# Kernel optimization log

Hardware: AMD Instinct MI355X
Metric: run time of the kernel (lower is better)

Reference implementation:

```python
import jax, jax.numpy as jnp
import numpy as np

BANDWIDTH = 1.0  # init kwarg: bandwidth; sphere mode -> var_s = gamma = bandwidth
LOG2PI = float(np.log(2.0 * np.pi))


def setup_inputs() -> dict:
    key = jax.random.key(0)
    k1, k2, k3, k4 = jax.random.split(key, 4)
    x = jax.random.normal(k1, (4096, 256), dtype=jnp.float32)
    y = jax.random.normal(k2, (4096, 128), dtype=jnp.float32)
    x_s = jax.random.normal(k3, (8192, 256), dtype=jnp.float32)
    y_s = jax.random.normal(k4, (8192, 128), dtype=jnp.float32)
    return {"x": x, "y": y, "x_s": x_s, "y_s": y_s}


def _sq_dists(a, b):
    # ||a_i - b_j||^2 via GEMM expansion: (batch, num_s)
    a2 = jnp.sum(a * a, axis=-1)[:, None]
    b2 = jnp.sum(b * b, axis=-1)[None, :]
    return a2 + b2 - 2.0 * jnp.einsum("bd,sd->bs", a, b)


def reference(x, y, x_s, y_s):
    x_dim = x.shape[-1]
    y_dim = y.shape[-1]
    var_s = BANDWIDTH
    gamma = BANDWIDTH
    logA_x = x_dim * (LOG2PI + jnp.log(jnp.float32(var_s)))
    logA_y = y_dim * (LOG2PI + jnp.log(jnp.float32(gamma)))

    sdx = _sq_dists(x, x_s) / var_s  # (batch, num_s)
    sdy = _sq_dists(y, y_s) / gamma  # (batch, num_s)

    E_log_pxy = jax.nn.logsumexp(-0.5 * (logA_x + logA_y + sdx + sdy), axis=-1)
    E_log_px = jax.nn.logsumexp(-0.5 * (logA_x + sdx), axis=-1)
    E_log_py = jax.nn.logsumexp(-0.5 * (logA_y + sdy), axis=-1)
    return jnp.mean(E_log_pxy - E_log_px - E_log_py)
```

## Files before the change

kernel.cpp:

```cpp
#include <hip/hip_runtime.h>
#include <hip/hip_bf16.h>
#include <stdint.h>

#define B_N 4096
#define S_N 8192
#define KX  256
#define KY  128
#define BM 128
#define BN 128

typedef __bf16 bf16x8 __attribute__((ext_vector_type(8)));
typedef float  f32x4  __attribute__((ext_vector_type(4)));

#define OFF_XH   ((size_t)0)
#define OFF_YH   ((size_t)2097152)
#define OFF_SXH  ((size_t)3145728)
#define OFF_SYH  ((size_t)7340032)
#define OFF_NX   ((size_t)9437184)
#define OFF_NY   (OFF_NX + 16384)
#define OFF_NSX  (OFF_NY + 16384)
#define OFF_NSY  (OFF_NSX + 32768)
#define OFF_PART (OFF_NSY + 32768)
#define OFF_BSUM (OFF_PART + (size_t)3*64*4096*2*4)

__device__ __forceinline__ void gl2lds16(const void* g, void* l) {
  typedef const __attribute__((address_space(1))) unsigned int* gp_t;
  typedef __attribute__((address_space(3))) unsigned int* lp_t;
  __builtin_amdgcn_global_load_lds((gp_t)g, (lp_t)l, 16, 0, 0);
}

__device__ __forceinline__ unsigned short f2bf(float f) {
  unsigned u = __builtin_bit_cast(unsigned, f);
  return (unsigned short)((u + 0x7fffu + ((u >> 16) & 1u)) >> 16);
}

__global__ __launch_bounds__(256) void conv_all(const float* __restrict__ x,
                                                const float* __restrict__ y,
                                                const float* __restrict__ xs,
                                                const float* __restrict__ ys,
                                                char* __restrict__ ws) {
  int b    = blockIdx.x;
  int wave = threadIdx.x >> 6;
  int lane = threadIdx.x & 63;
  const float* src; unsigned short* hi; float* nrm;
  int K, row;
  if (b < 1024) {
    src = x;  hi = (unsigned short*)(ws + OFF_XH);
    nrm = (float*)(ws + OFF_NX); K = 256; row = b * 4 + wave;
  } else if (b < 2048) {
    src = y;  hi = (unsigned short*)(ws + OFF_YH);
    nrm = (float*)(ws + OFF_NY); K = 128; row = (b - 1024) * 4 + wave;
  } else if (b < 4096) {
    src = xs; hi = (unsigned short*)(ws + OFF_SXH);
    nrm = (float*)(ws + OFF_NSX); K = 256; row = (b - 2048) * 4 + wave;
  } else {
    src = ys; hi = (unsigned short*)(ws + OFF_SYH);
    nrm = (float*)(ws + OFF_NSY); K = 128; row = (b - 4096) * 4 + wave;
  }
  float acc = 0.f;
  if (K == 256) {
    float4 v = ((const float4*)(src + (size_t)row * 256))[lane];
    float vv[4] = {v.x, v.y, v.z, v.w};
    ushort4 h4;
    unsigned short* hp = (unsigned short*)&h4;
    #pragma unroll
    for (int k = 0; k < 4; ++k) {
      hp[k] = f2bf(vv[k]);
      acc = fmaf(vv[k], vv[k], acc);
    }
    ((ushort4*)(hi + (size_t)row * 256))[lane] = h4;
  } else {
    float2 v = ((const float2*)(src + (size_t)row * 128))[lane];
    float vv[2] = {v.x, v.y};
    ushort2 h2;
    unsigned short* hp = (unsigned short*)&h2;
    #pragma unroll
    for (int k = 0; k < 2; ++k) {
      hp[k] = f2bf(vv[k]);
      acc = fmaf(vv[k], vv[k], acc);
    }
    ((ushort2*)(hi + (size_t)row * 128))[lane] = h2;
  }
  #pragma unroll
  for (int o = 32; o > 0; o >>= 1) acc += __shfl_down(acc, o);
  if (lane == 0) nrm[row] = acc;
}

__global__ __launch_bounds__(512, 4) void mie_main(const char* __restrict__ ws,
                                                   float* __restrict__ part) {
  __shared__ __align__(16) char smem[65536];

  const int tid  = threadIdx.x;
  const int lane = tid & 63;
  const int wave = tid >> 6;
  const int c    = lane & 15;
  const int q    = lane >> 4;
  const int wm   = wave >> 1;
  const int wn   = wave & 1;

  const int b     = blockIdx.x;
  const int xcd   = b & 7;
  const int w     = b >> 3;
  const int bm_t  = w & 31;
  const int sn_t  = xcd * 8 + (w >> 5);
  const int bm0   = bm_t * BM;
  const int sn0   = sn_t * BN;

  const char* xh  = ws + OFF_XH;
  const char* yh  = ws + OFF_YH;
  const char* sxh = ws + OFF_SXH;
  const char* syh = ws + OFF_SYH;
  const float* nx  = (const float*)(ws + OFF_NX);
  const float* ny  = (const float*)(ws + OFF_NY);
  const float* nsx = (const float*)(ws + OFF_NSX);
  const float* nsy = (const float*)(ws + OFF_NSY);

  const int r  = tid >> 2;
  const int sg = (tid & 3) ^ ((r >> 1) & 3);
  const char* aXp = xh  + (size_t)(bm0 + r) * 512 + sg * 16;
  const char* aYp = yh  + (size_t)(bm0 + r) * 256 + sg * 16;
  const char* bXp = sxh + (size_t)(sn0 + r) * 512 + sg * 16;
  const char* bYp = syh + (size_t)(sn0 + r) * 256 + sg * 16;
  char* sdst = smem + wave * 1024;

  const int slot  = (q ^ ((c >> 1) & 3)) * 16;
  const int aoff0 = (wm * 32 +  0 + c) * 64 + slot;
  const int aoff1 = (wm * 32 + 16 + c) * 64 + slot;
  const int boff0 = (wn * 64 +  0 + c) * 64 + slot;
  const int boff1 = (wn * 64 + 16 + c) * 64 + slot;
  const int boff2 = (wn * 64 + 32 + c) * 64 + slot;
  const int boff3 = (wn * 64 + 48 + c) * 64 + slot;

  f32x4 accx[2][4], accy[2][4];
  #pragma unroll
  for (int i = 0; i < 2; ++i)
    #pragma unroll
    for (int j = 0; j < 4; ++j) {
      accx[i][j] = (f32x4){0.f,0.f,0.f,0.f};
      accy[i][j] = (f32x4){0.f,0.f,0.f,0.f};
    }

#define STAGE(kc) do {                                                      \
    const char* _sa; const char* _sb;                                       \
    if ((kc) < 8) { _sa = aXp + (kc) * 64;       _sb = bXp + (kc) * 64; }   \
    else          { _sa = aYp + ((kc) - 8) * 64; _sb = bYp + ((kc) - 8) * 64; } \
    char* _d = sdst + ((kc) & 3) * 16384;                                   \
    gl2lds16(_sa, _d);                                                      \
    gl2lds16(_sb, _d + 8192);                                               \
  } while (0)

#define MFMA8(ACC, A0, A1, B0, B1, B2, B3) do {                                   \
    ACC[0][0] = __builtin_amdgcn_mfma_f32_16x16x32_bf16(A0, B0, ACC[0][0], 0,0,0); \
    ACC[0][1] = __builtin_amdgcn_mfma_f32_16x16x32_bf16(A0, B1, ACC[0][1], 0,0,0); \
    ACC[0][2] = __builtin_amdgcn_mfma_f32_16x16x32_bf16(A0, B2, ACC[0][2], 0,0,0); \
    ACC[0][3] = __builtin_amdgcn_mfma_f32_16x16x32_bf16(A0, B3, ACC[0][3], 0,0,0); \
    ACC[1][0] = __builtin_amdgcn_mfma_f32_16x16x32_bf16(A1, B0, ACC[1][0], 0,0,0); \
    ACC[1][1] = __builtin_amdgcn_mfma_f32_16x16x32_bf16(A1, B1, ACC[1][1], 0,0,0); \
    ACC[1][2] = __builtin_amdgcn_mfma_f32_16x16x32_bf16(A1, B2, ACC[1][2], 0,0,0); \
    ACC[1][3] = __builtin_amdgcn_mfma_f32_16x16x32_bf16(A1, B3, ACC[1][3], 0,0,0); \
  } while (0)

#define ITER(kc, vm, ACC) do {                                              \
    asm volatile("s_waitcnt vmcnt(" #vm ")" ::: "memory");                  \
    __builtin_amdgcn_s_barrier();                                           \
    asm volatile("" ::: "memory");                                          \
    const char* _base = smem + ((kc) & 3) * 16384;                          \
    bf16x8 _A0 = *(const bf16x8*)(_base + aoff0);                           \
    bf16x8 _A1 = *(const bf16x8*)(_base + aoff1);                           \
    bf16x8 _B0 = *(const bf16x8*)(_base + 8192 + boff0);                    \
    bf16x8 _B1 = *(const bf16x8*)(_base + 8192 + boff1);                    \
    bf16x8 _B2 = *(const bf16x8*)(_base + 8192 + boff2);                    \
    bf16x8 _B3 = *(const bf16x8*)(_base + 8192 + boff3);                    \
    if ((kc) + 3 < 12) STAGE((kc) + 3);                                     \
    __builtin_amdgcn_s_setprio(1);                                          \
    MFMA8(ACC, _A0, _A1, _B0, _B1, _B2, _B3);                               \
    __builtin_amdgcn_s_setprio(0);                                          \
  } while (0)

  STAGE(0); STAGE(1); STAGE(2);

  ITER(0, 4, accx);  ITER(1, 4, accx);  ITER(2, 4, accx);  ITER(3, 4, accx);
  ITER(4, 4, accx);  ITER(5, 4, accx);  ITER(6, 4, accx);  ITER(7, 4, accx);
  ITER(8, 4, accy);  ITER(9, 4, accy);  ITER(10, 2, accy); ITER(11, 0, accy);

#undef ITER
#undef MFMA8
#undef STAGE

  float hxv[2][4], hyv[2][4];
  #pragma unroll
  for (int i = 0; i < 2; ++i)
    #pragma unroll
    for (int rr4 = 0; rr4 < 4; ++rr4) {
      int rr = bm0 + wm * 32 + i * 16 + q * 4 + rr4;
      hxv[i][rr4] = -0.5f * nx[rr];
      hyv[i][rr4] = -0.5f * ny[rr];
    }
  float hsxv[4], hsyv[4];
  #pragma unroll
  for (int j = 0; j < 4; ++j) {
    int cc = sn0 + wn * 64 + j * 16 + c;
    hsxv[j] = -0.5f * nsx[cc];
    hsyv[j] = -0.5f * nsy[cc];
  }

  float2* xch2 = (float2*)smem;
  #pragma unroll
  for (int i = 0; i < 2; ++i) {
    #pragma unroll
    for (int rr4 = 0; rr4 < 4; ++rr4) {
      float vx[4], vy[4];
      #pragma unroll
      for (int j = 0; j < 4; ++j) {
        vx[j] = accx[i][j][rr4] + hxv[i][rr4] + hsxv[j];
        vy[j] = accy[i][j][rr4] + hyv[i][rr4] + hsyv[j];
      }
      int rl = wm * 32 + i * 16 + q * 4 + rr4;
      #pragma unroll
      for (int st = 0; st < 3; ++st) {
        float v0 = (st == 0) ? vx[0] + vy[0] : (st == 1 ? vx[0] : vy[0]);
        float v1 = (st == 0) ? vx[1] + vy[1] : (st == 1 ? vx[1] : vy[1]);
        float v2 = (st == 0) ? vx[2] + vy[2] : (st == 1 ? vx[2] : vy[2]);
        float v3 = (st == 0) ? vx[3] + vy[3] : (st == 1 ? vx[3] : vy[3]);
        float m = fmaxf(fmaxf(v0, v1), fmaxf(v2, v3));
        float s = __expf(v0 - m) + __expf(v1 - m) + __expf(v2 - m) + __expf(v3 - m);
        float mo = __shfl_xor(m, 8);
        float so = __shfl_xor(s, 8);
        float nm = fmaxf(m, mo);
        float ns = s * __expf(m - nm) + so * __expf(mo - nm);
        if (c < 8) xch2[(st * 128 + rl) * 16 + wn * 8 + c] = (float2){nm, ns};
      }
    }
  }
  __syncthreads();

  if (tid < 384) {
    int st = tid >> 7;
    int rl = tid & 127;
    const float2* row = xch2 + (st * 128 + rl) * 16;
    int p0 = rl & 15;
    float2 a = row[p0];
    float m = a.x, s = a.y;
    #pragma unroll
    for (int p = 1; p < 16; ++p) {
      float2 e = row[(p0 + p) & 15];
      float nm = fmaxf(m, e.x);
      s = s * __expf(m - nm) + e.y * __expf(e.x - nm);
      m = nm;
    }
    size_t idx = ((size_t)st * 64 + sn_t) * B_N + (bm0 + rl);
    ((float2*)part)[idx] = (float2){m, s};
  }
}

__global__ __launch_bounds__(256) void fin1(const float* __restrict__ part,
                                            float* __restrict__ bsum) {
  __shared__ float2 lds[3][4][64];
  int tid  = threadIdx.x;
  int wave = tid >> 6;
  int lane = tid & 63;
  int row  = blockIdx.x * 64 + lane;
  #pragma unroll
  for (int j = 0; j < 3; ++j) {
    float m = -__builtin_inff(), s = 0.f;
    #pragma unroll
    for (int pp = 0; pp < 16; ++pp) {
      int p = wave * 16 + pp;
      float2 a = ((const float2*)part)[((size_t)j * 64 + p) * B_N + row];
      float nm = fmaxf(m, a.x);
      s = s * __expf(m - nm) + a.y * __expf(a.x - nm);
      m = nm;
    }
    lds[j][wave][lane] = (float2){m, s};
  }
  __syncthreads();
  if (wave == 0) {
    float v[3];
    #pragma unroll
    for (int j = 0; j < 3; ++j) {
      float m = -__builtin_inff(), s = 0.f;
      #pragma unroll
      for (int u = 0; u < 4; ++u) {
        float2 a = lds[j][u][lane];
        float nm = fmaxf(m, a.x);
        s = s * __expf(m - nm) + a.y * __expf(a.x - nm);
        m = nm;
      }
      v[j] = m + __logf(s);
    }
    float local = v[0] - v[1] - v[2];
    #pragma unroll
    for (int o = 32; o > 0; o >>= 1) local += __shfl_down(local, o);
    if (lane == 0) bsum[blockIdx.x] = local;
  }
}

__global__ void fin2(const float* __restrict__ bsum, float* __restrict__ out) {
  int t = threadIdx.x;
  float a = bsum[t];
  #pragma unroll
  for (int o = 32; o > 0; o >>= 1) a += __shfl_down(a, o);
  if (t == 0) out[0] = a * (1.0f / (float)B_N);
}

extern "C" void kernel_launch(void* const* d_in, const int* in_sizes, int n_in,
                              void* d_out, int out_size, void* d_ws, size_t ws_size,
                              hipStream_t stream) {
  (void)in_sizes; (void)n_in; (void)out_size; (void)ws_size;
  const float* x  = (const float*)d_in[0];
  const float* y  = (const float*)d_in[1];
  const float* xs = (const float*)d_in[2];
  const float* ys = (const float*)d_in[3];
  char* ws = (char*)d_ws;

  conv_all<<<6144, 256, 0, stream>>>(x, y, xs, ys, ws);
  mie_main<<<2048, 512, 0, stream>>>(ws, (float*)(ws + OFF_PART));
  fin1<<<B_N / 64, 256, 0, stream>>>((const float*)(ws + OFF_PART), (float*)(ws + OFF_BSUM));
  fin2<<<1, 64, 0, stream>>>((const float*)(ws + OFF_BSUM), (float*)d_out);
}
```

Baseline: 130.5 us.

## Load A fragments straight to registers and fuse final reductions via atomic last-block

The A operand is now loaded from global memory directly into registers with one-step lookahead instead of being staged through LDS. This cuts LDS to 48KB and halves the global-to-LDS traffic per stage. The two finishing kernels are replaced by a last-block-done pattern: atomic counters per row panel pick the final block, which merges the partial logsumexp values, and a global counter does the final mean. This removes two kernel launches at the cost of atomics, fences and more per-thread global loads that are not shared across waves.

```diff
diff --git a/kernel.cpp b/kernel.cpp
--- a/kernel.cpp
+++ b/kernel.cpp
@@ -42,6 +42,7 @@
   int b    = blockIdx.x;
   int wave = threadIdx.x >> 6;
   int lane = threadIdx.x & 63;
+  if (b == 0 && threadIdx.x < 34) ((unsigned*)(ws + OFF_BSUM))[threadIdx.x] = 0u;
   const float* src; unsigned short* hi; float* nrm;
   int K, row;
   if (b < 1024) {
@@ -86,9 +87,11 @@
   if (lane == 0) nrm[row] = acc;
 }
 
-__global__ __launch_bounds__(512, 4) void mie_main(const char* __restrict__ ws,
-                                                   float* __restrict__ part) {
-  __shared__ __align__(16) char smem[65536];
+__global__ __launch_bounds__(512, 4) void mie_main(char* __restrict__ ws,
+                                                   float* __restrict__ part,
+                                                   float* __restrict__ out) {
+  __shared__ __align__(16) char smem[49152];
+  __shared__ int lastFlag;
 
   const int tid  = threadIdx.x;
   const int lane = tid & 63;
@@ -114,18 +117,20 @@
   const float* ny  = (const float*)(ws + OFF_NY);
   const float* nsx = (const float*)(ws + OFF_NSX);
   const float* nsy = (const float*)(ws + OFF_NSY);
+  unsigned* cnt_panel = (unsigned*)(ws + OFF_BSUM);
+  unsigned* done      = cnt_panel + 32;
+  float*    fsum      = (float*)(cnt_panel + 33);
 
   const int r  = tid >> 2;
   const int sg = (tid & 3) ^ ((r >> 1) & 3);
-  const char* aXp = xh  + (size_t)(bm0 + r) * 512 + sg * 16;
-  const char* aYp = yh  + (size_t)(bm0 + r) * 256 + sg * 16;
   const char* bXp = sxh + (size_t)(sn0 + r) * 512 + sg * 16;
   const char* bYp = syh + (size_t)(sn0 + r) * 256 + sg * 16;
   char* sdst = smem + wave * 1024;
 
+  const char* aXb = xh + (size_t)(bm0 + wm * 32 + c) * 512 + q * 16;
+  const char* aYb = yh + (size_t)(bm0 + wm * 32 + c) * 256 + q * 16;
+
   const int slot  = (q ^ ((c >> 1) & 3)) * 16;
-  const int aoff0 = (wm * 32 +  0 + c) * 64 + slot;
-  const int aoff1 = (wm * 32 + 16 + c) * 64 + slot;
   const int boff0 = (wn * 64 +  0 + c) * 64 + slot;
   const int boff1 = (wn * 64 + 16 + c) * 64 + slot;
   const int boff2 = (wn * 64 + 32 + c) * 64 + slot;
@@ -140,13 +145,21 @@
       accy[i][j] = (f32x4){0.f,0.f,0.f,0.f};
     }
 
-#define STAGE(kc) do {                                                      \
-    const char* _sa; const char* _sb;                                       \
-    if ((kc) < 8) { _sa = aXp + (kc) * 64;       _sb = bXp + (kc) * 64; }   \
-    else          { _sa = aYp + ((kc) - 8) * 64; _sb = bYp + ((kc) - 8) * 64; } \
-    char* _d = sdst + ((kc) & 3) * 16384;                                   \
-    gl2lds16(_sa, _d);                                                      \
-    gl2lds16(_sb, _d + 8192);                                               \
+  bf16x8 AH[2][2];
+
+#define LOADA(kc, P) do {                                                   \
+    if ((kc) < 8) {                                                         \
+      AH[P][0] = *(const bf16x8*)(aXb + (kc) * 64);                         \
+      AH[P][1] = *(const bf16x8*)(aXb + 8192 + (kc) * 64);                  \
+    } else {                                                                \
+      AH[P][0] = *(const bf16x8*)(aYb + ((kc) - 8) * 64);                   \
+      AH[P][1] = *(const bf16x8*)(aYb + 4096 + ((kc) - 8) * 64);            \
+    }                                                                       \
+  } while (0)
+
+#define STAGEB(kc) do {                                                     \
+    const char* _sb = ((kc) < 8) ? (bXp + (kc) * 64) : (bYp + ((kc) - 8) * 64); \
+    gl2lds16(_sb, sdst + ((kc) & 3) * 8192);                                \
   } while (0)
 
 #define MFMA8(ACC, A0, A1, B0, B1, B2, B3) do {                                   \
@@ -164,28 +177,33 @@
     asm volatile("s_waitcnt vmcnt(" #vm ")" ::: "memory");                  \
     __builtin_amdgcn_s_barrier();                                           \
     asm volatile("" ::: "memory");                                          \
-    const char* _base = smem + ((kc) & 3) * 16384;                          \
-    bf16x8 _A0 = *(const bf16x8*)(_base + aoff0);                           \
-    bf16x8 _A1 = *(const bf16x8*)(_base + aoff1);                           \
-    bf16x8 _B0 = *(const bf16x8*)(_base + 8192 + boff0);                    \
-    bf16x8 _B1 = *(const bf16x8*)(_base + 8192 + boff1);                    \
-    bf16x8 _B2 = *(const bf16x8*)(_base + 8192 + boff2);                    \
-    bf16x8 _B3 = *(const bf16x8*)(_base + 8192 + boff3);                    \
-    if ((kc) + 3 < 12) STAGE((kc) + 3);                                     \
+    const char* _b = smem + ((kc) & 3) * 8192;                              \
+    bf16x8 _B0 = *(const bf16x8*)(_b + boff0);                              \
+    bf16x8 _B1 = *(const bf16x8*)(_b + boff1);                              \
+    bf16x8 _B2 = *(const bf16x8*)(_b + boff2);                              \
+    bf16x8 _B3 = *(const bf16x8*)(_b + boff3);                              \
+    if ((kc) + 1 < 12) LOADA((kc) + 1, (((kc) + 1) & 1));                   \
+    asm volatile("" ::: "memory");                                          \
+    if ((kc) + 3 < 12) STAGEB((kc) + 3);                                    \
     __builtin_amdgcn_s_setprio(1);                                          \
-    MFMA8(ACC, _A0, _A1, _B0, _B1, _B2, _B3);                               \
+    MFMA8(ACC, AH[(kc) & 1][0], AH[(kc) & 1][1], _B0, _B1, _B2, _B3);       \
     __builtin_amdgcn_s_setprio(0);                                          \
   } while (0)
 
-  STAGE(0); STAGE(1); STAGE(2);
-
-  ITER(0, 4, accx);  ITER(1, 4, accx);  ITER(2, 4, accx);  ITER(3, 4, accx);
-  ITER(4, 4, accx);  ITER(5, 4, accx);  ITER(6, 4, accx);  ITER(7, 4, accx);
-  ITER(8, 4, accy);  ITER(9, 4, accy);  ITER(10, 2, accy); ITER(11, 0, accy);
+  LOADA(0, 0);
+  asm volatile("" ::: "memory");
+  STAGEB(0); STAGEB(1); STAGEB(2);
+
+  ITER(0, 2, accx);  ITER(1, 4, accx);  ITER(2, 6, accx);  ITER(3, 6, accx);
+  ITER(4, 6, accx);  ITER(5, 6, accx);  ITER(6, 6, accx);  ITER(7, 6, accx);
+  ITER(8, 6, accy);  ITER(9, 6, accy);  ITER(10, 5, accy); ITER(11, 4, accy);
 
 #undef ITER
 #undef MFMA8
-#undef STAGE
+#undef STAGEB
+#undef LOADA
+
+  __syncthreads();
 
   float hxv[2][4], hyv[2][4];
   #pragma unroll
@@ -251,56 +269,51 @@
     size_t idx = ((size_t)st * 64 + sn_t) * B_N + (bm0 + rl);
     ((float2*)part)[idx] = (float2){m, s};
   }
-}
-
-__global__ __launch_bounds__(256) void fin1(const float* __restrict__ part,
-                                            float* __restrict__ bsum) {
-  __shared__ float2 lds[3][4][64];
-  int tid  = threadIdx.x;
-  int wave = tid >> 6;
-  int lane = tid & 63;
-  int row  = blockIdx.x * 64 + lane;
-  #pragma unroll
-  for (int j = 0; j < 3; ++j) {
-    float m = -__builtin_inff(), s = 0.f;
-    #pragma unroll
-    for (int pp = 0; pp < 16; ++pp) {
-      int p = wave * 16 + pp;
-      float2 a = ((const float2*)part)[((size_t)j * 64 + p) * B_N + row];
-      float nm = fmaxf(m, a.x);
-      s = s * __expf(m - nm) + a.y * __expf(a.x - nm);
-      m = nm;
-    }
-    lds[j][wave][lane] = (float2){m, s};
-  }
+
+  __threadfence();
   __syncthreads();
-  if (wave == 0) {
-    float v[3];
-    #pragma unroll
-    for (int j = 0; j < 3; ++j) {
+  if (tid == 0) {
+    unsigned old = atomicAdd(cnt_panel + bm_t, 1u);
+    lastFlag = (old == 63u) ? 1 : 0;
+  }
+  __syncthreads();
+  if (lastFlag) {
+    __threadfence();
+    float* vtab = (float*)smem;
+    if (tid < 384) {
+      int st = tid >> 7;
+      int rl = tid & 127;
+      const float2* pp = (const float2*)part + (size_t)st * 64 * B_N + (bm0 + rl);
       float m = -__builtin_inff(), s = 0.f;
-      #pragma unroll
-      for (int u = 0; u < 4; ++u) {
-        float2 a = lds[j][u][lane];
-        float nm = fmaxf(m, a.x);
-        s = s * __expf(m - nm) + a.y * __expf(a.x - nm);
+      #pragma unroll 8
+      for (int p = 0; p < 64; ++p) {
+        float2 e = pp[(size_t)p * B_N];
+        float nm = fmaxf(m, e.x);
+        s = s * __expf(m - nm) + e.y * __expf(e.x - nm);
         m = nm;
       }
-      v[j] = m + __logf(s);
-    }
-    float local = v[0] - v[1] - v[2];
-    #pragma unroll
-    for (int o = 32; o > 0; o >>= 1) local += __shfl_down(local, o);
-    if (lane == 0) bsum[blockIdx.x] = local;
-  }
-}
-
-__global__ void fin2(const float* __restrict__ bsum, float* __restrict__ out) {
-  int t = threadIdx.x;
-  float a = bsum[t];
-  #pragma unroll
-  for (int o = 32; o > 0; o >>= 1) a += __shfl_down(a, o);
-  if (t == 0) out[0] = a * (1.0f / (float)B_N);
+      vtab[st * 128 + rl] = m + __logf(s);
+    }
+    __syncthreads();
+    if (tid < 128) {
+      float local = vtab[tid] - vtab[128 + tid] - vtab[256 + tid];
+      #pragma unroll
+      for (int o = 32; o > 0; o >>= 1) local += __shfl_down(local, o);
+      if ((tid & 63) == 0) vtab[384 + (tid >> 6)] = local;
+    }
+    __syncthreads();
+    if (tid == 0) {
+      float ps = vtab[384] + vtab[385];
+      atomicAdd(fsum, ps);
+      __threadfence();
+      unsigned od = atomicAdd(done, 1u);
+      if (od == 31u) {
+        __threadfence();
+        float tot = atomicAdd(fsum, 0.0f);
+        out[0] = tot * (1.0f / (float)B_N);
+      }
+    }
+  }
 }
 
 extern "C" void kernel_launch(void* const* d_in, const int* in_sizes, int n_in,
@@ -314,7 +327,5 @@
   char* ws = (char*)d_ws;
 
   conv_all<<<6144, 256, 0, stream>>>(x, y, xs, ys, ws);
-  mie_main<<<2048, 512, 0, stream>>>(ws, (float*)(ws + OFF_PART));
-  fin1<<<B_N / 64, 256, 0, stream>>>((const float*)(ws + OFF_PART), (float*)(ws + OFF_BSUM));
-  fin2<<<1, 64, 0, stream>>>((const float*)(ws + OFF_BSUM), (float*)d_out);
-}
+  mie_main<<<2048, 512, 0, stream>>>(ws, (float*)(ws + OFF_PART), (float*)d_out);
+}
```

Result: slower. 423.9 us (+224.9%).

## Load A fragments directly from global into registers, stage only B through LDS

Applied to the files above, without the earlier changes.

A-operand fragments are now read from global memory straight into registers, double-buffered one k-step ahead, instead of being staged through shared memory. Only the B tile goes through the LDS ring buffer, which shrinks shared memory from 64KB to 48KB and removes the A-side LDS reads. The vmcnt wait counts are retuned for the mixed direct loads and async LDS copies, and a barrier is added before the epilogue. The trade-off is that each wave issues its own redundant global loads of A rows (the two waves sharing wm read the same data), and the wait counts must stay correct for the new load ordering.

```diff
diff --git a/kernel.cpp b/kernel.cpp
--- a/kernel.cpp
+++ b/kernel.cpp
@@ -88,7 +88,7 @@
 
 __global__ __launch_bounds__(512, 4) void mie_main(const char* __restrict__ ws,
                                                    float* __restrict__ part) {
-  __shared__ __align__(16) char smem[65536];
+  __shared__ __align__(16) char smem[49152];
 
   const int tid  = threadIdx.x;
   const int lane = tid & 63;
@@ -117,15 +117,14 @@
 
   const int r  = tid >> 2;
   const int sg = (tid & 3) ^ ((r >> 1) & 3);
-  const char* aXp = xh  + (size_t)(bm0 + r) * 512 + sg * 16;
-  const char* aYp = yh  + (size_t)(bm0 + r) * 256 + sg * 16;
   const char* bXp = sxh + (size_t)(sn0 + r) * 512 + sg * 16;
   const char* bYp = syh + (size_t)(sn0 + r) * 256 + sg * 16;
   char* sdst = smem + wave * 1024;
 
+  const char* aXb = xh + (size_t)(bm0 + wm * 32 + c) * 512 + q * 16;
+  const char* aYb = yh + (size_t)(bm0 + wm * 32 + c) * 256 + q * 16;
+
   const int slot  = (q ^ ((c >> 1) & 3)) * 16;
-  const int aoff0 = (wm * 32 +  0 + c) * 64 + slot;
-  const int aoff1 = (wm * 32 + 16 + c) * 64 + slot;
   const int boff0 = (wn * 64 +  0 + c) * 64 + slot;
   const int boff1 = (wn * 64 + 16 + c) * 64 + slot;
   const int boff2 = (wn * 64 + 32 + c) * 64 + slot;
@@ -140,13 +139,21 @@
       accy[i][j] = (f32x4){0.f,0.f,0.f,0.f};
     }
 
-#define STAGE(kc) do {                                                      \
-    const char* _sa; const char* _sb;                                       \
-    if ((kc) < 8) { _sa = aXp + (kc) * 64;       _sb = bXp + (kc) * 64; }   \
-    else          { _sa = aYp + ((kc) - 8) * 64; _sb = bYp + ((kc) - 8) * 64; } \
-    char* _d = sdst + ((kc) & 3) * 16384;                                   \
-    gl2lds16(_sa, _d);                                                      \
-    gl2lds16(_sb, _d + 8192);                                               \
+  bf16x8 AH[2][2];
+
+#define LOADA(kc, P) do {                                                   \
+    if ((kc) < 8) {                                                         \
+      AH[P][0] = *(const bf16x8*)(aXb + (kc) * 64);                         \
+      AH[P][1] = *(const bf16x8*)(aXb + 8192 + (kc) * 64);                  \
+    } else {                                                                \
+      AH[P][0] = *(const bf16x8*)(aYb + ((kc) - 8) * 64);                   \
+      AH[P][1] = *(const bf16x8*)(aYb + 4096 + ((kc) - 8) * 64);            \
+    }                                                                       \
+  } while (0)
+
+#define STAGEB(kc) do {                                                     \
+    const char* _sb = ((kc) < 8) ? (bXp + (kc) * 64) : (bYp + ((kc) - 8) * 64); \
+    gl2lds16(_sb, sdst + ((kc) & 3) * 8192);                                \
   } while (0)
 
 #define MFMA8(ACC, A0, A1, B0, B1, B2, B3) do {                                   \
@@ -164,28 +171,33 @@
     asm volatile("s_waitcnt vmcnt(" #vm ")" ::: "memory");                  \
     __builtin_amdgcn_s_barrier();                                           \
     asm volatile("" ::: "memory");                                          \
-    const char* _base = smem + ((kc) & 3) * 16384;                          \
-    bf16x8 _A0 = *(const bf16x8*)(_base + aoff0);                           \
-    bf16x8 _A1 = *(const bf16x8*)(_base + aoff1);                           \
-    bf16x8 _B0 = *(const bf16x8*)(_base + 8192 + boff0);                    \
-    bf16x8 _B1 = *(const bf16x8*)(_base + 8192 + boff1);                    \
-    bf16x8 _B2 = *(const bf16x8*)(_base + 8192 + boff2);                    \
-    bf16x8 _B3 = *(const bf16x8*)(_base + 8192 + boff3);                    \
-    if ((kc) + 3 < 12) STAGE((kc) + 3);                                     \
+    const char* _b = smem + ((kc) & 3) * 8192;                              \
+    bf16x8 _B0 = *(const bf16x8*)(_b + boff0);                              \
+    bf16x8 _B1 = *(const bf16x8*)(_b + boff1);                              \
+    bf16x8 _B2 = *(const bf16x8*)(_b + boff2);                              \
+    bf16x8 _B3 = *(const bf16x8*)(_b + boff3);                              \
+    if ((kc) + 1 < 12) LOADA((kc) + 1, (((kc) + 1) & 1));                   \
+    asm volatile("" ::: "memory");                                          \
+    if ((kc) + 3 < 12) STAGEB((kc) + 3);                                    \
     __builtin_amdgcn_s_setprio(1);                                          \
-    MFMA8(ACC, _A0, _A1, _B0, _B1, _B2, _B3);                               \
+    MFMA8(ACC, AH[(kc) & 1][0], AH[(kc) & 1][1], _B0, _B1, _B2, _B3);       \
     __builtin_amdgcn_s_setprio(0);                                          \
   } while (0)
 
-  STAGE(0); STAGE(1); STAGE(2);
-
-  ITER(0, 4, accx);  ITER(1, 4, accx);  ITER(2, 4, accx);  ITER(3, 4, accx);
-  ITER(4, 4, accx);  ITER(5, 4, accx);  ITER(6, 4, accx);  ITER(7, 4, accx);
-  ITER(8, 4, accy);  ITER(9, 4, accy);  ITER(10, 2, accy); ITER(11, 0, accy);
+  LOADA(0, 0);
+  asm volatile("" ::: "memory");
+  STAGEB(0); STAGEB(1); STAGEB(2);
+
+  ITER(0, 2, accx);  ITER(1, 4, accx);  ITER(2, 6, accx);  ITER(3, 6, accx);
+  ITER(4, 6, accx);  ITER(5, 6, accx);  ITER(6, 6, accx);  ITER(7, 6, accx);
+  ITER(8, 6, accy);  ITER(9, 6, accy);  ITER(10, 5, accy); ITER(11, 4, accy);
 
 #undef ITER
 #undef MFMA8
-#undef STAGE
+#undef STAGEB
+#undef LOADA
+
+  __syncthreads();
 
   float hxv[2][4], hyv[2][4];
   #pragma unroll
```

Result: slower. 144.5 us (+10.8%).
